# Optimization experiments

Hardware: AMD Instinct MI355X
Metric: run time of the kernel (lower is better)

## Reference

```python
import jax, jax.numpy as jnp
import numpy as np

C_WEIGHT = 0.005  # 'c' hyperparameter

def _psi(v):
    return jnp.sign(v) * jnp.log1p(jnp.abs(v))

def setup_inputs() -> dict:
    key = jax.random.key(0)
    ks = jax.random.split(key, 16)
    B, P, C = 64, 128, 72
    s = lambda fan_in: 1.0 / np.sqrt(fan_in)
    return {
        'x': jax.random.normal(ks[0], (B, P, 4), dtype=jnp.float32),
        'h': jax.random.normal(ks[1], (B, P, C), dtype=jnp.float32),
        'We1': jax.random.normal(ks[2], (2 * C + 2, 72), dtype=jnp.float32) * s(2 * C + 2),
        'be1': jnp.zeros((72,), dtype=jnp.float32),
        'We2': jax.random.normal(ks[3], (72, 72), dtype=jnp.float32) * s(72),
        'be2': jnp.zeros((72,), dtype=jnp.float32),
        'Wm': jax.random.normal(ks[4], (72, 1), dtype=jnp.float32) * s(72),
        'bm': jnp.zeros((1,), dtype=jnp.float32),
        'Wh1': jax.random.normal(ks[5], (C + 72, 72), dtype=jnp.float32) * s(C + 72),
        'bh1': jnp.zeros((72,), dtype=jnp.float32),
        'Wh2': jax.random.normal(ks[6], (72, 72), dtype=jnp.float32) * s(72),
        'bh2': jnp.zeros((72,), dtype=jnp.float32),
        'Wx': jax.random.normal(ks[7], (72, 1), dtype=jnp.float32) * s(72),
    }

def reference(x, h, We1, be1, We2, be2, Wm, bm, Wh1, bh1, Wh2, bh2, Wx):
    B, P, _ = x.shape
    # pairwise Minkowski invariants: take(...,0)*2 - sum == t^2 - |vec|^2
    x1 = x[:, :, None, :]  # (B,P,1,4)
    x2 = x[:, None, :, :]  # (B,1,P,4)
    d2 = jnp.square(x1 - x2)                      # (B,P,P,4)
    norms = 2.0 * d2[..., 0] - d2.sum(axis=-1)    # (B,P,P)
    z = x1 * x2
    prods = 2.0 * z[..., 0] - z.sum(axis=-1)      # (B,P,P)
    norms = _psi(norms)[..., None]                # use_psi=True
    prods = _psi(prods)[..., None]
    H = h.shape[-1]
    h1 = jnp.broadcast_to(h[:, :, None, :], (B, P, P, H))
    h2 = jnp.broadcast_to(h[:, None, :, :], (B, P, P, H))
    feat = jnp.concatenate([h1, h2, norms, prods], axis=-1)  # (B,P,P,2H+2)
    # phi_e: two Dense+ReLU
    m = jax.nn.relu(feat @ We1 + be1)
    m = jax.nn.relu(m @ We2 + be2)                # (B,P,P,72)
    # phi_m: Dense(1) + sigmoid
    w = jax.nn.sigmoid(m @ Wm + bm)               # (B,P,P,1)
    wm = jnp.sum(w * m, axis=2)                   # (B,P,72)
    # phi_h: Dense+ReLU, Dense; residual add
    g = jax.nn.relu(jnp.concatenate([h, wm], axis=-1) @ Wh1 + bh1)
    dh = g @ Wh2 + bh2
    h_out = h + dh
    # phi_x: Dense(1, no bias); x update
    phi_x = m @ Wx                                # (B,P,P,1)
    x_out = x + C_WEIGHT * jnp.mean(phi_x * x[:, None, :, :], axis=2)
    return (h_out, x_out)
```

## Files before the change

kernel.cpp:

```cpp
#include <hip/hip_runtime.h>
#include <hip/hip_bf16.h>
#include <math.h>

#define B_ 64
#define P_ 128
#define C_ 72
#define PADC 80
#define BCS 88
#define IT 8

typedef __attribute__((ext_vector_type(8))) _Float16 half8v;
typedef __attribute__((ext_vector_type(2))) _Float16 half2v;
typedef __attribute__((ext_vector_type(4))) float f32x4;
typedef __attribute__((ext_vector_type(2))) float f32x2;
typedef __attribute__((ext_vector_type(4))) unsigned int u32x4;

#define FRAG_WE2  0
#define FRAG_WE1A (15 * 64)
#define FRAG_WE1B (30 * 64)
#define FRAG_WH1  (45 * 64)
#define FRAG_WH2  (70 * 64)
#define NFRAG 85

__device__ __forceinline__ float psi_f(float v) {
    float a = fabsf(v);
    return copysignf(__logf(1.0f + a), v);
}
template <int CTRL>
__device__ __forceinline__ float dpp_add(float v) {
    int s = __builtin_amdgcn_update_dpp(0, __builtin_bit_cast(int, v), CTRL, 0xF, 0xF, true);
    return v + __builtin_bit_cast(float, s);
}
__device__ __forceinline__ float red16(float v) {
    v = dpp_add<0xB1>(v);
    v = dpp_add<0x4E>(v);
    v = dpp_add<0x141>(v);
    v = dpp_add<0x140>(v);
    return v;
}
__device__ __forceinline__ half8v cvt8(const float* p) {
    f32x4 a = *(const f32x4*)p;
    f32x4 b = *(const f32x4*)(p + 4);
    half8v r = {(_Float16)a[0], (_Float16)a[1], (_Float16)a[2], (_Float16)a[3],
                (_Float16)b[0], (_Float16)b[1], (_Float16)b[2], (_Float16)b[3]};
    return r;
}

__global__ __launch_bounds__(64) void setup_kernel(
    const float* __restrict__ We1, const float* __restrict__ be1,
    const float* __restrict__ We2, const float* __restrict__ be2,
    const float* __restrict__ Wh1, const float* __restrict__ bh1,
    const float* __restrict__ Wh2, const float* __restrict__ bh2,
    half8v* __restrict__ frags)
{
    const int bid = blockIdx.x;
    const int l = threadIdx.x;
    const int c16 = l & 15, g = l >> 4;

    const float* W;
    const float* bias;
    int kmax, rel;
    if (bid < 15)      { W = We2;            bias = be2;     kmax = 72;  rel = bid; }
    else if (bid < 30) { W = We1;            bias = nullptr; kmax = 72;  rel = bid - 15; }
    else if (bid < 45) { W = We1 + 72 * C_;  bias = be1;     kmax = 72;  rel = bid - 30; }
    else if (bid < 70) { W = Wh1;            bias = bh1;     kmax = 144; rel = bid - 45; }
    else               { W = Wh2;            bias = bh2;     kmax = 72;  rel = bid - 70; }
    const int kt = rel / 5, nt = rel - 5 * kt;
    const int n = nt * 16 + c16;

    half8v f = {};
    if (n < C_) {
        #pragma unroll
        for (int jj = 0; jj < 8; ++jj) {
            int k = kt * 32 + g * 8 + jj;
            float w = 0.f;
            if (k < kmax) w = W[k * C_ + n];
            else if (k == kmax && bias) w = bias[n];
            f[jj] = (_Float16)w;
        }
    }
    frags[bid * 64 + l] = f;
}

__global__ __launch_bounds__(64) void pre_kernel(
    const float* __restrict__ h, const half8v* __restrict__ frags,
    _Float16* __restrict__ Ah, _Float16* __restrict__ Bch)
{
    const int l = threadIdx.x, c16 = l & 15, g = l >> 4;
    const int sel = blockIdx.x & 1;
    const int m0 = (blockIdx.x >> 1) * 16;

    const float* hrow = h + (m0 + c16) * C_;
    half8v a0 = cvt8(hrow + g * 8);
    half8v a1 = cvt8(hrow + 32 + g * 8);
    half8v a2 = {};
    if (g == 0) a2 = cvt8(hrow + 64);
    else if (g == 1) a2[0] = (_Float16)1.0f;

    const half8v* F = frags + (sel ? FRAG_WE1B : FRAG_WE1A);
    f32x4 acc[5] = {};
    #pragma unroll
    for (int kt = 0; kt < 3; ++kt) {
        half8v a = (kt == 0) ? a0 : (kt == 1 ? a1 : a2);
        #pragma unroll
        for (int nt = 0; nt < 5; ++nt)
            acc[nt] = __builtin_amdgcn_mfma_f32_16x16x32_f16(a, F[(kt * 5 + nt) * 64 + l], acc[nt], 0, 0, 0);
    }
    _Float16* dst = sel ? Bch : Ah;
    #pragma unroll
    for (int nt = 0; nt < 5; ++nt) {
        int n = nt * 16 + c16;
        if (n < C_) {
            #pragma unroll
            for (int r = 0; r < 4; ++r)
                dst[(m0 + 4 * g + r) * PADC + n] = (_Float16)acc[nt][r];
        }
    }
}

__global__ __launch_bounds__(256, 2) void edge_kernel(
    const float* __restrict__ x, const _Float16* __restrict__ Ah,
    const _Float16* __restrict__ Bch, const float* __restrict__ We1,
    const half8v* __restrict__ frags,
    const float* __restrict__ Wm, const float* __restrict__ bm,
    const float* __restrict__ Wx,
    float* __restrict__ wm_out, float* __restrict__ xacc_out)
{
    __shared__ __align__(16) _Float16 A_s[IT][PADC];
    __shared__ __align__(16) _Float16 Bc_s[P_][BCS];
    __shared__ __align__(16) float xj_s[P_][4];

    const int b  = blockIdx.x >> 4;
    const int it = blockIdx.x & 15;
    const int t  = threadIdx.x;
    const int wv = t >> 6;
    const int l  = t & 63;
    const int c16 = l & 15;
    const int g   = l >> 4;

    {
        const unsigned int* Asrc = (const unsigned int*)(Ah + (b * P_ + it * IT) * PADC);
        for (int idx = t; idx < IT * PADC / 2; idx += 256)
            ((unsigned int*)A_s)[idx] = Asrc[idx];
        for (int cidx = t; cidx < P_ * 10; cidx += 256) {
            int r = cidx / 10, c = cidx - r * 10;
            *(u32x4*)&Bc_s[r][c * 8] = ((const u32x4*)(Bch + (b * P_ + r) * PADC))[c];
        }
        for (int idx = t; idx < P_ * 4; idx += 256)
            ((float*)xj_s)[idx] = x[b * P_ * 4 + idx];
    }

    const float* w1g = We1 + 144 * C_;
    const float* w2g = We1 + 145 * C_;
    half8v w1a = cvt8(w1g + g * 8);
    half8v w1b = cvt8(w1g + 32 + g * 8);
    half8v w1c = cvt8(w1g + 64);
    half8v w2a = cvt8(w2g + g * 8);
    half8v w2b = cvt8(w2g + 32 + g * 8);
    half8v w2c = cvt8(w2g + 64);

    half8v Wf[3][5];
    #pragma unroll
    for (int kt = 0; kt < 3; ++kt)
        #pragma unroll
        for (int nt = 0; nt < 5; ++nt)
            Wf[kt][nt] = frags[FRAG_WE2 + (kt * 5 + nt) * 64 + l];

    half2v WmWx[5][4];
    #pragma unroll
    for (int nt = 0; nt < 5; ++nt)
        #pragma unroll
        for (int r = 0; r < 4; ++r) {
            int ch = nt * 16 + 4 * g + r;
            bool ok = ch < C_;
            WmWx[nt][r][0] = (_Float16)(ok ? Wm[ch] : 0.f);
            WmWx[nt][r][1] = (_Float16)(ok ? Wx[ch] : 0.f);
        }
    const float bm0 = bm[0];
    const f32x4 zero4 = {0.f, 0.f, 0.f, 0.f};

    __syncthreads();

    #pragma unroll 1
    for (int ii = 0; ii < 2; ++ii) {
        const int iloc = wv * 2 + ii;
        const int i = it * IT + iloc;
        const int node_i = b * P_ + i;
        const f32x4 xi = *(const f32x4*)&xj_s[i][0];

        half8v ava = *(const half8v*)&A_s[iloc][g * 8];
        half8v avb = *(const half8v*)&A_s[iloc][32 + g * 8];
        half8v avc = *(const half8v*)&A_s[iloc][64];

        f32x4 wmacc[5] = {};
        f32x4 xacc = {0.f, 0.f, 0.f, 0.f};

        #pragma unroll 1
        for (int jt = 0; jt < 8; ++jt) {
            const int j = jt * 16 + c16;
            const f32x4 xjv = *(const f32x4*)&xj_s[j][0];
            float d0 = xi[0] - xjv[0], d1 = xi[1] - xjv[1];
            float d2 = xi[2] - xjv[2], d3 = xi[3] - xjv[3];
            float nn = d0 * d0 - d1 * d1 - d2 * d2 - d3 * d3;
            float pp = xi[0] * xjv[0] - xi[1] * xjv[1] - xi[2] * xjv[2] - xi[3] * xjv[3];
            _Float16 nh = (_Float16)psi_f(nn);
            _Float16 ph = (_Float16)psi_f(pp);
            half8v n8 = {nh, nh, nh, nh, nh, nh, nh, nh};
            half8v p8 = {ph, ph, ph, ph, ph, ph, ph, ph};
            half8v zero8 = {};

            auto mk = [&](half8v av, const _Float16* bp, half8v w1, half8v w2) -> half8v {
                half8v v = av + *(const half8v*)bp;
                v = __builtin_elementwise_fma(w1, n8, v);
                v = __builtin_elementwise_fma(w2, p8, v);
                return __builtin_elementwise_max(v, zero8);
            };
            half8v af0 = mk(ava, &Bc_s[j][g * 8],      w1a, w2a);
            half8v af1 = mk(avb, &Bc_s[j][32 + g * 8], w1b, w2b);
            half8v af2 = {};
            if (g == 0) af2 = mk(avc, &Bc_s[j][64], w1c, w2c);
            else if (g == 1) af2[0] = (_Float16)1.0f;

            f32x4 acc[5] = {};
            #pragma unroll
            for (int nt = 0; nt < 5; ++nt)
                acc[nt] = __builtin_amdgcn_mfma_f32_16x16x32_f16(Wf[0][nt], af0, acc[nt], 0, 0, 0);
            #pragma unroll
            for (int nt = 0; nt < 5; ++nt)
                acc[nt] = __builtin_amdgcn_mfma_f32_16x16x32_f16(Wf[1][nt], af1, acc[nt], 0, 0, 0);
            #pragma unroll
            for (int nt = 0; nt < 5; ++nt)
                acc[nt] = __builtin_amdgcn_mfma_f32_16x16x32_f16(Wf[2][nt], af2, acc[nt], 0, 0, 0);

            float wd = 0.f, pd = 0.f;
            #pragma unroll
            for (int nt = 0; nt < 5; ++nt) {
                f32x4 m2q = __builtin_elementwise_max(acc[nt], zero4);
                acc[nt] = m2q;
                #pragma unroll
                for (int r = 0; r < 4; ++r) {
                    wd = fmaf(m2q[r], (float)WmWx[nt][r][0], wd);
                    pd = fmaf(m2q[r], (float)WmWx[nt][r][1], pd);
                }
            }
            wd += __shfl_xor(wd, 16, 64);
            pd += __shfl_xor(pd, 16, 64);
            wd += __shfl_xor(wd, 32, 64);
            pd += __shfl_xor(pd, 32, 64);

            float w_ = __builtin_amdgcn_rcpf(1.f + __expf(-(wd + bm0)));
            f32x4 w4 = {w_, w_, w_, w_};
            #pragma unroll
            for (int nt = 0; nt < 5; ++nt)
                wmacc[nt] = __builtin_elementwise_fma(w4, acc[nt], wmacc[nt]);
            f32x4 pd4 = {pd, pd, pd, pd};
            xacc = __builtin_elementwise_fma(pd4, xjv, xacc);
        }

        #pragma unroll
        for (int nt = 0; nt < 5; ++nt)
            #pragma unroll
            for (int r = 0; r < 4; ++r)
                wmacc[nt][r] = red16(wmacc[nt][r]);
        #pragma unroll
        for (int q = 0; q < 4; ++q) xacc[q] = red16(xacc[q]);

        if (c16 == 0) {
            #pragma unroll
            for (int nt = 0; nt < 5; ++nt)
                #pragma unroll
                for (int r = 0; r < 4; ++r) {
                    int ch = nt * 16 + 4 * g + r;
                    if (ch < C_) wm_out[node_i * C_ + ch] = wmacc[nt][r];
                }
        }
        if (l == 0)
            *(f32x4*)&xacc_out[node_i * 4] = xacc;
    }
}

__global__ __launch_bounds__(64) void node_kernel(
    const float* __restrict__ x, const float* __restrict__ h,
    const half8v* __restrict__ frags,
    const float* __restrict__ wm, const float* __restrict__ xacc,
    float* __restrict__ hout, float* __restrict__ xout)
{
    __shared__ _Float16 g_s[16][BCS];
    const int l = threadIdx.x, c16 = l & 15, g = l >> 4;
    const int m0 = blockIdx.x * 16;

    const float* hrow  = h  + (m0 + c16) * C_;
    const float* wmrow = wm + (m0 + c16) * C_;

    half8v a[5];
    #pragma unroll
    for (int kt = 0; kt < 5; ++kt) {
        int k = kt * 32 + g * 8;
        half8v v = {};
        if (k < C_) v = cvt8(hrow + k);
        else if (k < 144) v = cvt8(wmrow + (k - C_));
        else if (k == 144) v[0] = (_Float16)1.0f;
        a[kt] = v;
    }
    f32x4 acc1[5] = {};
    #pragma unroll
    for (int kt = 0; kt < 5; ++kt)
        #pragma unroll
        for (int nt = 0; nt < 5; ++nt)
            acc1[nt] = __builtin_amdgcn_mfma_f32_16x16x32_f16(
                a[kt], frags[FRAG_WH1 + (kt * 5 + nt) * 64 + l], acc1[nt], 0, 0, 0);

    #pragma unroll
    for (int nt = 0; nt < 5; ++nt) {
        int n = nt * 16 + c16;
        #pragma unroll
        for (int r = 0; r < 4; ++r)
            g_s[4 * g + r][n] = (_Float16)fmaxf(acc1[nt][r], 0.f);
    }
    half8v b0 = *(const half8v*)&g_s[c16][g * 8];
    half8v b1 = *(const half8v*)&g_s[c16][32 + g * 8];
    half8v b2 = {};
    if (g == 0) b2 = *(const half8v*)&g_s[c16][64];
    else if (g == 1) b2[0] = (_Float16)1.0f;

    f32x4 acc2[5] = {};
    #pragma unroll
    for (int kt = 0; kt < 3; ++kt) {
        half8v aa = (kt == 0) ? b0 : (kt == 1 ? b1 : b2);
        #pragma unroll
        for (int nt = 0; nt < 5; ++nt)
            acc2[nt] = __builtin_amdgcn_mfma_f32_16x16x32_f16(
                aa, frags[FRAG_WH2 + (kt * 5 + nt) * 64 + l], acc2[nt], 0, 0, 0);
    }
    #pragma unroll
    for (int nt = 0; nt < 5; ++nt) {
        int n = nt * 16 + c16;
        if (n < C_) {
            #pragma unroll
            for (int r = 0; r < 4; ++r) {
                int row = m0 + 4 * g + r;
                hout[row * C_ + n] = h[row * C_ + n] + acc2[nt][r];
            }
        }
    }
    {
        int row = m0 + (l >> 2), d = l & 3;
        xout[row * 4 + d] = x[row * 4 + d] + 0.005f * (xacc[row * 4 + d] * (1.0f / 128.f));
    }
}

extern "C" void kernel_launch(void* const* d_in, const int* in_sizes, int n_in,
                              void* d_out, int out_size, void* d_ws, size_t ws_size,
                              hipStream_t stream) {
    const float* x   = (const float*)d_in[0];
    const float* h   = (const float*)d_in[1];
    const float* We1 = (const float*)d_in[2];
    const float* be1 = (const float*)d_in[3];
    const float* We2 = (const float*)d_in[4];
    const float* be2 = (const float*)d_in[5];
    const float* Wm  = (const float*)d_in[6];
    const float* bm  = (const float*)d_in[7];
    const float* Wh1 = (const float*)d_in[8];
    const float* bh1 = (const float*)d_in[9];
    const float* Wh2 = (const float*)d_in[10];
    const float* bh2 = (const float*)d_in[11];
    const float* Wx  = (const float*)d_in[12];

    const int NNODE = B_ * P_;
    _Float16* Ah  = (_Float16*)d_ws;
    _Float16* Bch = Ah + NNODE * PADC;
    float* wm   = (float*)(Bch + NNODE * PADC);
    float* xacc = wm + NNODE * C_;
    half8v* frags = (half8v*)(xacc + NNODE * 4);

    float* hout = (float*)d_out;
    float* xout = hout + NNODE * C_;

    setup_kernel<<<NFRAG, 64, 0, stream>>>(We1, be1, We2, be2, Wh1, bh1, Wh2, bh2, frags);
    pre_kernel<<<NNODE / 16 * 2, 64, 0, stream>>>(h, frags, Ah, Bch);
    edge_kernel<<<B_ * 16, 256, 0, stream>>>(x, Ah, Bch, We1, frags,
                                             Wm, bm, Wx, wm, xacc);
    node_kernel<<<NNODE / 16, 64, 0, stream>>>(x, h, frags, wm, xacc, hout, xout);
}
```

Measured before the change: 62.12 us.

## Process two i-rows per wave together to reuse Bc loads and interleave MFMAs

The edge kernel now fuses the two sequential i-iterations per wave into one j-loop that handles both rows A and B at once. Each Bc_s and xj_s load is shared across the two rows, and the two independent MFMA chains are interleaved to hide MFMA latency. The Wm/Wx weights move from fp16 to fp32 with packed f32x2 FMAs, and the min-2-blocks occupancy hint is dropped to make room for the higher register pressure. The risk is fewer resident waves per CU, or spilling.

Result: slower. 78.25 us (+26.0%).

```diff
diff --git a/kernel.cpp b/kernel.cpp
--- a/kernel.cpp
+++ b/kernel.cpp
@@ -118,7 +118,7 @@
     }
 }
 
-__global__ __launch_bounds__(256, 2) void edge_kernel(
+__global__ __launch_bounds__(256) void edge_kernel(
     const float* __restrict__ x, const _Float16* __restrict__ Ah,
     const _Float16* __restrict__ Bch, const float* __restrict__ We1,
     const half8v* __restrict__ frags,
@@ -166,116 +166,171 @@
         for (int nt = 0; nt < 5; ++nt)
             Wf[kt][nt] = frags[FRAG_WE2 + (kt * 5 + nt) * 64 + l];
 
-    half2v WmWx[5][4];
+    f32x2 WmWx[5][4];
     #pragma unroll
     for (int nt = 0; nt < 5; ++nt)
         #pragma unroll
         for (int r = 0; r < 4; ++r) {
             int ch = nt * 16 + 4 * g + r;
             bool ok = ch < C_;
-            WmWx[nt][r][0] = (_Float16)(ok ? Wm[ch] : 0.f);
-            WmWx[nt][r][1] = (_Float16)(ok ? Wx[ch] : 0.f);
+            WmWx[nt][r][0] = ok ? Wm[ch] : 0.f;
+            WmWx[nt][r][1] = ok ? Wx[ch] : 0.f;
         }
     const float bm0 = bm[0];
     const f32x4 zero4 = {0.f, 0.f, 0.f, 0.f};
 
     __syncthreads();
 
+    const int i0 = it * IT + wv * 2;
+    const int node0 = b * P_ + i0;
+    const f32x4 xiA = *(const f32x4*)&xj_s[i0][0];
+    const f32x4 xiB = *(const f32x4*)&xj_s[i0 + 1][0];
+
+    half8v avA0 = *(const half8v*)&A_s[wv * 2][g * 8];
+    half8v avA1 = *(const half8v*)&A_s[wv * 2][32 + g * 8];
+    half8v avA2 = *(const half8v*)&A_s[wv * 2][64];
+    half8v avB0 = *(const half8v*)&A_s[wv * 2 + 1][g * 8];
+    half8v avB1 = *(const half8v*)&A_s[wv * 2 + 1][32 + g * 8];
+    half8v avB2 = *(const half8v*)&A_s[wv * 2 + 1][64];
+
+    f32x4 wmaccA[5] = {}, wmaccB[5] = {};
+    f32x4 xaccA = {0.f, 0.f, 0.f, 0.f}, xaccB = {0.f, 0.f, 0.f, 0.f};
+
     #pragma unroll 1
-    for (int ii = 0; ii < 2; ++ii) {
-        const int iloc = wv * 2 + ii;
-        const int i = it * IT + iloc;
-        const int node_i = b * P_ + i;
-        const f32x4 xi = *(const f32x4*)&xj_s[i][0];
-
-        half8v ava = *(const half8v*)&A_s[iloc][g * 8];
-        half8v avb = *(const half8v*)&A_s[iloc][32 + g * 8];
-        half8v avc = *(const half8v*)&A_s[iloc][64];
-
-        f32x4 wmacc[5] = {};
-        f32x4 xacc = {0.f, 0.f, 0.f, 0.f};
-
-        #pragma unroll 1
-        for (int jt = 0; jt < 8; ++jt) {
-            const int j = jt * 16 + c16;
-            const f32x4 xjv = *(const f32x4*)&xj_s[j][0];
-            float d0 = xi[0] - xjv[0], d1 = xi[1] - xjv[1];
-            float d2 = xi[2] - xjv[2], d3 = xi[3] - xjv[3];
-            float nn = d0 * d0 - d1 * d1 - d2 * d2 - d3 * d3;
-            float pp = xi[0] * xjv[0] - xi[1] * xjv[1] - xi[2] * xjv[2] - xi[3] * xjv[3];
-            _Float16 nh = (_Float16)psi_f(nn);
-            _Float16 ph = (_Float16)psi_f(pp);
-            half8v n8 = {nh, nh, nh, nh, nh, nh, nh, nh};
-            half8v p8 = {ph, ph, ph, ph, ph, ph, ph, ph};
-            half8v zero8 = {};
-
-            auto mk = [&](half8v av, const _Float16* bp, half8v w1, half8v w2) -> half8v {
-                half8v v = av + *(const half8v*)bp;
-                v = __builtin_elementwise_fma(w1, n8, v);
-                v = __builtin_elementwise_fma(w2, p8, v);
-                return __builtin_elementwise_max(v, zero8);
-            };
-            half8v af0 = mk(ava, &Bc_s[j][g * 8],      w1a, w2a);
-            half8v af1 = mk(avb, &Bc_s[j][32 + g * 8], w1b, w2b);
-            half8v af2 = {};
-            if (g == 0) af2 = mk(avc, &Bc_s[j][64], w1c, w2c);
-            else if (g == 1) af2[0] = (_Float16)1.0f;
-
-            f32x4 acc[5] = {};
+    for (int jt = 0; jt < 8; ++jt) {
+        const int j = jt * 16 + c16;
+        const f32x4 xjv = *(const f32x4*)&xj_s[j][0];
+        half8v bc0 = *(const half8v*)&Bc_s[j][g * 8];
+        half8v bc1 = *(const half8v*)&Bc_s[j][32 + g * 8];
+        half8v bc2 = *(const half8v*)&Bc_s[j][64];
+        half8v zero8 = {};
+
+        float dA0 = xiA[0] - xjv[0], dA1 = xiA[1] - xjv[1];
+        float dA2 = xiA[2] - xjv[2], dA3 = xiA[3] - xjv[3];
+        float nnA = dA0 * dA0 - dA1 * dA1 - dA2 * dA2 - dA3 * dA3;
+        float ppA = xiA[0] * xjv[0] - xiA[1] * xjv[1] - xiA[2] * xjv[2] - xiA[3] * xjv[3];
+        _Float16 nhA = (_Float16)psi_f(nnA);
+        _Float16 phA = (_Float16)psi_f(ppA);
+        half8v n8A = {nhA, nhA, nhA, nhA, nhA, nhA, nhA, nhA};
+        half8v p8A = {phA, phA, phA, phA, phA, phA, phA, phA};
+
+        float dB0 = xiB[0] - xjv[0], dB1 = xiB[1] - xjv[1];
+        float dB2 = xiB[2] - xjv[2], dB3 = xiB[3] - xjv[3];
+        float nnB = dB0 * dB0 - dB1 * dB1 - dB2 * dB2 - dB3 * dB3;
+        float ppB = xiB[0] * xjv[0] - xiB[1] * xjv[1] - xiB[2] * xjv[2] - xiB[3] * xjv[3];
+        _Float16 nhB = (_Float16)psi_f(nnB);
+        _Float16 phB = (_Float16)psi_f(ppB);
+        half8v n8B = {nhB, nhB, nhB, nhB, nhB, nhB, nhB, nhB};
+        half8v p8B = {phB, phB, phB, phB, phB, phB, phB, phB};
+
+        auto mk = [&](half8v av, half8v bv, half8v w1, half8v w2,
+                      half8v n8, half8v p8) -> half8v {
+            half8v v = av + bv;
+            v = __builtin_elementwise_fma(w1, n8, v);
+            v = __builtin_elementwise_fma(w2, p8, v);
+            return __builtin_elementwise_max(v, zero8);
+        };
+        half8v afA0 = mk(avA0, bc0, w1a, w2a, n8A, p8A);
+        half8v afA1 = mk(avA1, bc1, w1b, w2b, n8A, p8A);
+        half8v afB0 = mk(avB0, bc0, w1a, w2a, n8B, p8B);
+        half8v afB1 = mk(avB1, bc1, w1b, w2b, n8B, p8B);
+        half8v afA2 = {}, afB2 = {};
+        if (g == 0) {
+            afA2 = mk(avA2, bc2, w1c, w2c, n8A, p8A);
+            afB2 = mk(avB2, bc2, w1c, w2c, n8B, p8B);
+        } else if (g == 1) {
+            afA2[0] = (_Float16)1.0f;
+            afB2[0] = (_Float16)1.0f;
+        }
+
+        f32x4 accA[5] = {}, accB[5] = {};
+        #pragma unroll
+        for (int nt = 0; nt < 5; ++nt) {
+            accA[nt] = __builtin_amdgcn_mfma_f32_16x16x32_f16(Wf[0][nt], afA0, accA[nt], 0, 0, 0);
+            accB[nt] = __builtin_amdgcn_mfma_f32_16x16x32_f16(Wf[0][nt], afB0, accB[nt], 0, 0, 0);
+        }
+        #pragma unroll
+        for (int nt = 0; nt < 5; ++nt) {
+            accA[nt] = __builtin_amdgcn_mfma_f32_16x16x32_f16(Wf[1][nt], afA1, accA[nt], 0, 0, 0);
+            accB[nt] = __builtin_amdgcn_mfma_f32_16x16x32_f16(Wf[1][nt], afB1, accB[nt], 0, 0, 0);
+        }
+        #pragma unroll
+        for (int nt = 0; nt < 5; ++nt) {
+            accA[nt] = __builtin_amdgcn_mfma_f32_16x16x32_f16(Wf[2][nt], afA2, accA[nt], 0, 0, 0);
+            accB[nt] = __builtin_amdgcn_mfma_f32_16x16x32_f16(Wf[2][nt], afB2, accB[nt], 0, 0, 0);
+        }
+
+        f32x2 wdpdA = {0.f, 0.f}, wdpdB = {0.f, 0.f};
+        #pragma unroll
+        for (int nt = 0; nt < 5; ++nt) {
+            f32x4 mA = __builtin_elementwise_max(accA[nt], zero4);
+            f32x4 mB = __builtin_elementwise_max(accB[nt], zero4);
+            accA[nt] = mA;
+            accB[nt] = mB;
             #pragma unroll
-            for (int nt = 0; nt < 5; ++nt)
-                acc[nt] = __builtin_amdgcn_mfma_f32_16x16x32_f16(Wf[0][nt], af0, acc[nt], 0, 0, 0);
+            for (int r = 0; r < 4; ++r) {
+                f32x2 vA = {mA[r], mA[r]};
+                f32x2 vB = {mB[r], mB[r]};
+                wdpdA = __builtin_elementwise_fma(vA, WmWx[nt][r], wdpdA);
+                wdpdB = __builtin_elementwise_fma(vB, WmWx[nt][r], wdpdB);
+            }
+        }
+        {
+            f32x2 sA, sB;
+            sA[0] = __shfl_xor(wdpdA[0], 16, 64);
+            sB[0] = __shfl_xor(wdpdB[0], 16, 64);
+            sA[1] = __shfl_xor(wdpdA[1], 16, 64);
+            sB[1] = __shfl_xor(wdpdB[1], 16, 64);
+            wdpdA += sA; wdpdB += sB;
+            sA[0] = __shfl_xor(wdpdA[0], 32, 64);
+            sB[0] = __shfl_xor(wdpdB[0], 32, 64);
+            sA[1] = __shfl_xor(wdpdA[1], 32, 64);
+            sB[1] = __shfl_xor(wdpdB[1], 32, 64);
+            wdpdA += sA; wdpdB += sB;
+        }
+        float wA = __builtin_amdgcn_rcpf(1.f + __expf(-(wdpdA[0] + bm0)));
+        float wB = __builtin_amdgcn_rcpf(1.f + __expf(-(wdpdB[0] + bm0)));
+        f32x4 w4A = {wA, wA, wA, wA};
+        f32x4 w4B = {wB, wB, wB, wB};
+        #pragma unroll
+        for (int nt = 0; nt < 5; ++nt) {
+            wmaccA[nt] = __builtin_elementwise_fma(w4A, accA[nt], wmaccA[nt]);
+            wmaccB[nt] = __builtin_elementwise_fma(w4B, accB[nt], wmaccB[nt]);
+        }
+        f32x4 pdA = {wdpdA[1], wdpdA[1], wdpdA[1], wdpdA[1]};
+        f32x4 pdB = {wdpdB[1], wdpdB[1], wdpdB[1], wdpdB[1]};
+        xaccA = __builtin_elementwise_fma(pdA, xjv, xaccA);
+        xaccB = __builtin_elementwise_fma(pdB, xjv, xaccB);
+    }
+
+    #pragma unroll
+    for (int nt = 0; nt < 5; ++nt)
+        #pragma unroll
+        for (int r = 0; r < 4; ++r) {
+            wmaccA[nt][r] = red16(wmaccA[nt][r]);
+            wmaccB[nt][r] = red16(wmaccB[nt][r]);
+        }
+    #pragma unroll
+    for (int q = 0; q < 4; ++q) {
+        xaccA[q] = red16(xaccA[q]);
+        xaccB[q] = red16(xaccB[q]);
+    }
+
+    if (c16 == 0) {
+        #pragma unroll
+        for (int nt = 0; nt < 5; ++nt)
             #pragma unroll
-            for (int nt = 0; nt < 5; ++nt)
-                acc[nt] = __builtin_amdgcn_mfma_f32_16x16x32_f16(Wf[1][nt], af1, acc[nt], 0, 0, 0);
-            #pragma unroll
-            for (int nt = 0; nt < 5; ++nt)
-                acc[nt] = __builtin_amdgcn_mfma_f32_16x16x32_f16(Wf[2][nt], af2, acc[nt], 0, 0, 0);
-
-            float wd = 0.f, pd = 0.f;
-            #pragma unroll
-            for (int nt = 0; nt < 5; ++nt) {
-                f32x4 m2q = __builtin_elementwise_max(acc[nt], zero4);
-                acc[nt] = m2q;
-                #pragma unroll
-                for (int r = 0; r < 4; ++r) {
-                    wd = fmaf(m2q[r], (float)WmWx[nt][r][0], wd);
-                    pd = fmaf(m2q[r], (float)WmWx[nt][r][1], pd);
+            for (int r = 0; r < 4; ++r) {
+                int ch = nt * 16 + 4 * g + r;
+                if (ch < C_) {
+                    wm_out[node0 * C_ + ch] = wmaccA[nt][r];
+                    wm_out[(node0 + 1) * C_ + ch] = wmaccB[nt][r];
                 }
             }
-            wd += __shfl_xor(wd, 16, 64);
-            pd += __shfl_xor(pd, 16, 64);
-            wd += __shfl_xor(wd, 32, 64);
-            pd += __shfl_xor(pd, 32, 64);
-
-            float w_ = __builtin_amdgcn_rcpf(1.f + __expf(-(wd + bm0)));
-            f32x4 w4 = {w_, w_, w_, w_};
-            #pragma unroll
-            for (int nt = 0; nt < 5; ++nt)
-                wmacc[nt] = __builtin_elementwise_fma(w4, acc[nt], wmacc[nt]);
-            f32x4 pd4 = {pd, pd, pd, pd};
-            xacc = __builtin_elementwise_fma(pd4, xjv, xacc);
-        }
-
-        #pragma unroll
-        for (int nt = 0; nt < 5; ++nt)
-            #pragma unroll
-            for (int r = 0; r < 4; ++r)
-                wmacc[nt][r] = red16(wmacc[nt][r]);
-        #pragma unroll
-        for (int q = 0; q < 4; ++q) xacc[q] = red16(xacc[q]);
-
-        if (c16 == 0) {
-            #pragma unroll
-            for (int nt = 0; nt < 5; ++nt)
-                #pragma unroll
-                for (int r = 0; r < 4; ++r) {
-                    int ch = nt * 16 + 4 * g + r;
-                    if (ch < C_) wm_out[node_i * C_ + ch] = wmacc[nt][r];
-                }
-        }
-        if (l == 0)
-            *(f32x4*)&xacc_out[node_i * 4] = xacc;
+    }
+    if (l == 0) {
+        *(f32x4*)&xacc_out[node0 * 4] = xaccA;
+        *(f32x4*)&xacc_out[(node0 + 1) * 4] = xaccB;
     }
 }
 
```
